# Performance work log

Measured on AMD Instinct MI355X. Metric: run time of the kernel, lower is better.

Reference implementation:

```python
import jax, jax.numpy as jnp
import numpy as np

PI = np.pi


def setup_inputs() -> dict:
    key = jax.random.key(0)
    ks = jax.random.split(key, 20)
    B, L, D = 2, 1024, 512
    TP = 16      # n_sets(4) * planes_per_set(4)
    PP = 16      # pos_planes
    MAXL = 8192
    sc = 1.0 / np.sqrt(D)
    return {
        "x": jax.random.normal(ks[0], (B, L, D), jnp.float32),
        "Wk": jax.random.normal(ks[1], (TP, D), jnp.float32) * sc,
        "bk": jnp.zeros((TP,), jnp.float32),
        "Wq": jax.random.normal(ks[2], (TP, D), jnp.float32) * sc,
        "bq": jnp.zeros((TP,), jnp.float32),
        "Wv": jax.random.normal(ks[3], (D, D), jnp.float32) * sc,
        "bv": jnp.zeros((D,), jnp.float32),
        "ln_g": jnp.ones((D,), jnp.float32),
        "ln_b": jnp.zeros((D,), jnp.float32),
        "Wo": jax.random.normal(ks[4], (D, D), jnp.float32) * sc,
        "bo": jnp.zeros((D,), jnp.float32),
        "set_w": jnp.ones((4,), jnp.float32),
        "pos_phases": jax.random.normal(ks[5], (MAXL, PP), jnp.float32) * PI,
        "pos_weight": jnp.ones((1,), jnp.float32),
        "Wg1": jax.random.normal(ks[6], (D // 2, D), jnp.float32) * sc,
        "bg1": jnp.zeros((D // 2,), jnp.float32),
        "Wg2": jax.random.normal(ks[7], (1, D // 2), jnp.float32) * np.sqrt(2.0 / D),
        "bg2": jnp.zeros((1,), jnp.float32),
    }


def reference(x, Wk, bk, Wq, bq, Wv, bv, ln_g, ln_b, Wo, bo,
              set_w, pos_phases, pos_weight, Wg1, bg1, Wg2, bg2):
    B, L, D = x.shape
    n_sets, pps = 4, 4

    # --- content phasor memory ---
    kp = jnp.tanh(x @ Wk.T + bk) * PI                       # [B,L,16]
    qp = jnp.tanh(x @ Wq.T + bq) * PI
    key_ph = jnp.exp(1j * kp).reshape(B, L, n_sets, pps)    # [B,L,S,P] c64
    qry_ph = jnp.exp(1j * qp).reshape(B, L, n_sets, pps)
    Vr = x @ Wv.T + bv                                       # [B,L,D]
    V = Vr.astype(jnp.complex64)

    bound = key_ph[..., None] * V[:, :, None, None, :]       # [B,L,S,P,D] c64
    mem = jnp.cumsum(bound, axis=1)                          # prefix-sum memory
    retr = (mem * jnp.conj(qry_ph)[..., None]).sum(axis=3).real   # [B,L,S,D]
    w = jax.nn.softmax(set_w)
    content = (retr * w[None, None, :, None]).sum(axis=2)    # [B,L,D]

    # --- positional cos/sin memory ---
    ph = pos_phases[:L]                                      # [L,PP]
    c = jnp.cos(ph)[None]                                    # [1,L,PP]
    s = jnp.sin(ph)[None]
    br = Vr[:, :, None, :] * c[..., None]                    # [B,L,PP,D]
    bi = Vr[:, :, None, :] * s[..., None]
    mr = jnp.cumsum(br, axis=1)
    mi = jnp.cumsum(bi, axis=1)
    pos = (mr * c[..., None] + mi * s[..., None]).sum(axis=2)  # [B,L,D]

    # --- gate, mix, normalize, output proj ---
    g = jax.nn.sigmoid(
        jax.nn.gelu(x @ Wg1.T + bg1, approximate=False) @ Wg2.T + bg2)  # [B,L,1]
    total = g * content + (1.0 - g) * jax.nn.sigmoid(pos_weight) * pos
    norm = jnp.sqrt(jnp.arange(1, L + 1, dtype=x.dtype) * pps)[None, :, None]
    t = total / norm
    mu = t.mean(-1, keepdims=True)
    var = ((t - mu) ** 2).mean(-1, keepdims=True)
    tn = (t - mu) / jnp.sqrt(var + 1e-5) * ln_g + ln_b
    return x + tn @ Wo.T + bo
```

## Files before the change

### kernel.cpp

```cpp
#include <hip/hip_runtime.h>
#include <math.h>

#define PI_F 3.14159265358979323846f
#define BB 2
#define LL 1024
#define NCH 64
#define CHUNK 32
#define NCHUNK (LL/CHUNK)
#define NW 1408
#define YH 384

typedef __attribute__((ext_vector_type(8))) short short8;
typedef __attribute__((ext_vector_type(4))) float floatx4;
typedef const __attribute__((address_space(1))) unsigned int cgu32;
typedef __attribute__((address_space(3))) unsigned int lu32;

__device__ __forceinline__ unsigned short f2bf(float f){
    unsigned u = __float_as_uint(f);
    unsigned r = (u + 0x7fff + ((u >> 16) & 1)) >> 16;
    return (unsigned short)r;
}

__global__ __launch_bounds__(128) void k_prep(
    const float* __restrict__ Wv, const float* __restrict__ Wg1,
    const float* __restrict__ Wk, const float* __restrict__ Wq,
    const float* __restrict__ Wo,
    const float* __restrict__ bv, const float* __restrict__ bg1,
    const float* __restrict__ bk, const float* __restrict__ bq,
    const float* __restrict__ bo, const float* __restrict__ x,
    unsigned short* __restrict__ Wb, float* __restrict__ bcat,
    unsigned short* __restrict__ xb)
{
    const int bid = blockIdx.x, tid = threadIdx.x;
    if (bid < NW){
        const int n = bid;
        const float* src = (n<512) ? Wv  + (size_t)n*512
                         : (n<768) ? Wg1 + (size_t)(n-512)*512
                         : (n<784) ? Wk  + (size_t)(n-768)*512
                         : (n<800) ? Wq  + (size_t)(n-784)*512
                         : (n<896) ? (const float*)0
                                   : Wo  + (size_t)(n-896)*512;
        float4 v = make_float4(0.f,0.f,0.f,0.f);
        if (src) v = ((const float4*)src)[tid];
        ushort4 o; o.x=f2bf(v.x); o.y=f2bf(v.y); o.z=f2bf(v.z); o.w=f2bf(v.w);
        ((ushort4*)(Wb + (size_t)n*512))[tid] = o;
        if (tid == 0)
            bcat[n] = (n<512)?bv[n] : (n<768)?bg1[n-512] : (n<784)?bk[n-768]
                    : (n<800)?bq[n-784] : (n<896)?0.f : bo[n-896];
    } else {
        const size_t i = (size_t)(bid - NW)*128 + tid;
        float4 v = ((const float4*)x)[i];
        ushort4 o; o.x=f2bf(v.x); o.y=f2bf(v.y); o.z=f2bf(v.z); o.w=f2bf(v.w);
        ((ushort4*)xb)[i] = o;
    }
}

__device__ __forceinline__ void gemm64x64(
    const unsigned short* Ag, const unsigned short* Bg,
    short* As, short* Bs, int tid, floatx4 acc[2][2])
{
    const int lane = tid & 63, w = tid >> 6;
    const int wm = w & 1, wn = w >> 1;
    const int q = lane >> 4, m15 = lane & 15;
    for (int kt = 0; kt < 512; kt += 64) {
        __syncthreads();
        #pragma unroll
        for (int i = 0; i < 2; ++i) {
            const int rowbase = (w*2 + i) * 8;
            const int r  = rowbase + (lane >> 3);
            const int gb = (lane & 7) ^ (r & 7);
            const unsigned short* ga  = Ag + (size_t)r*512 + kt + gb*8;
            const unsigned short* gbp = Bg + (size_t)r*512 + kt + gb*8;
            __builtin_amdgcn_global_load_lds((cgu32*)(const void*)ga,
                                             (lu32*)(As + rowbase*64), 16, 0, 0);
            __builtin_amdgcn_global_load_lds((cgu32*)(const void*)gbp,
                                             (lu32*)(Bs + rowbase*64), 16, 0, 0);
        }
        __syncthreads();
        #pragma unroll
        for (int k32 = 0; k32 < 64; k32 += 32) {
            short8 af[2], bf[2];
            #pragma unroll
            for (int t = 0; t < 2; ++t) {
                const int ra  = 32*wm + 16*t + m15;
                const int sba = ((k32>>3) + q) ^ (ra & 7);
                af[t] = *(const short8*)(As + ra*64 + sba*8);
                const int rb  = 32*wn + 16*t + m15;
                const int sbb = ((k32>>3) + q) ^ (rb & 7);
                bf[t] = *(const short8*)(Bs + rb*64 + sbb*8);
            }
            #pragma unroll
            for (int mt = 0; mt < 2; ++mt)
                #pragma unroll
                for (int nt = 0; nt < 2; ++nt)
                    acc[mt][nt] = __builtin_amdgcn_mfma_f32_16x16x32_bf16(
                        af[mt], bf[nt], acc[mt][nt], 0, 0, 0);
        }
    }
}

__global__ __launch_bounds__(256) void kg1(
    const unsigned short* __restrict__ xb, const unsigned short* __restrict__ Wb,
    const float* __restrict__ bcat, unsigned short* __restrict__ Vt,
    float* __restrict__ Yh)
{
    __shared__ short As[64*64], Bs[64*64];
    const int tid = threadIdx.x;
    const int row0 = blockIdx.x*64, n0 = blockIdx.y*64;
    floatx4 acc[2][2];
    #pragma unroll
    for (int mt=0;mt<2;++mt)
        #pragma unroll
        for (int nt=0;nt<2;++nt) acc[mt][nt] = (floatx4){0.f,0.f,0.f,0.f};
    gemm64x64(xb + (size_t)row0*512, Wb + (size_t)n0*512, As, Bs, tid, acc);
    const int lane = tid & 63, w = tid >> 6;
    const int wm = w & 1, wn = w >> 1, q = lane >> 4, m15 = lane & 15;
    if (n0 < 512){
        const int b = row0 >> 10, lb = row0 & 1023;
        #pragma unroll
        for (int mt=0;mt<2;++mt)
            #pragma unroll
            for (int nt=0;nt<2;++nt){
                const int d = n0 + 32*wn + 16*nt + m15;
                const float bb = bcat[d];
                const int l0 = lb + 32*wm + 16*mt + q*4;
                ushort4 o;
                o.x = f2bf(acc[mt][nt][0] + bb);
                o.y = f2bf(acc[mt][nt][1] + bb);
                o.z = f2bf(acc[mt][nt][2] + bb);
                o.w = f2bf(acc[mt][nt][3] + bb);
                *(ushort4*)(Vt + ((size_t)(b*512 + d))*1024 + l0) = o;
            }
    } else {
        #pragma unroll
        for (int mt=0;mt<2;++mt)
            #pragma unroll
            for (int nt=0;nt<2;++nt){
                const int n = n0 + 32*wn + 16*nt + m15;
                const float bb = bcat[n];
                #pragma unroll
                for (int reg=0;reg<4;++reg){
                    const int m = row0 + 32*wm + 16*mt + q*4 + reg;
                    Yh[(size_t)m*YH + (n-512)] = acc[mt][nt][reg] + bb;
                }
            }
    }
}

__global__ __launch_bounds__(256) void k_act(
    const float* __restrict__ Yh, const float* __restrict__ Wg2,
    const float* __restrict__ bg2, const float* __restrict__ set_w,
    const float* __restrict__ pos_phases, const float* __restrict__ pos_weight,
    unsigned short* __restrict__ ab, unsigned short* __restrict__ Rb,
    unsigned short* __restrict__ aT)
{
    const int tid = threadIdx.x, lane = tid & 63, w = tid >> 6;
    const int row0 = blockIdx.x * 8;
    float s0=set_w[0], s1=set_w[1], s2=set_w[2], s3=set_w[3];
    float m = fmaxf(fmaxf(s0,s1), fmaxf(s2,s3));
    float e0=expf(s0-m), e1=expf(s1-m), e2=expf(s2-m), e3=expf(s3-m);
    float esum = e0+e1+e2+e3;
    float spw = 1.f/(1.f+expf(-pos_weight[0]));
    float b2 = bg2[0];
    #pragma unroll
    for (int rr=0;rr<2;++rr){
        int row = row0 + w + 4*rr;
        const float* yrow = Yh + (size_t)row*YH;
        float hs = 0.f;
        #pragma unroll
        for (int i=0;i<4;++i){
            float hv = yrow[lane + 64*i];
            float ge = 0.5f*hv*(1.f + erff(hv*0.70710678118f));
            hs += ge * Wg2[lane + 64*i];
        }
        #pragma unroll
        for (int off=32; off; off>>=1) hs += __shfl_xor(hs, off, 64);
        float g = 1.f/(1.f+expf(-(hs + b2)));
        if (lane < 16){
            int j = lane;
            int l = row & (LL-1);
            int b = row >> 10;
            float kang = PI_F*tanhf(yrow[256 + j]);
            float qang = PI_F*tanhf(yrow[272 + j]);
            float wsm = (j<4?e0: j<8?e1: j<12?e2: e3) / esum;
            float rnorm = 1.f/(2.f*sqrtf((float)(l+1)));
            float av[4], rv[4];
            av[0] = cosf(kang); av[1] = sinf(kang);
            float cw = g*wsm*rnorm;
            rv[0] = cw*cosf(qang); rv[1] = cw*sinf(qang);
            float ph = pos_phases[(size_t)l*16 + j];
            float pc = cosf(ph), ps = sinf(ph);
            av[2] = pc; av[3] = ps;
            float cp = (1.f-g)*spw*rnorm;
            rv[2] = cp*pc; rv[3] = cp*ps;
            unsigned short* arow = ab + (size_t)row*NCH;
            unsigned short* Rrow = Rb + (size_t)row*NCH;
            #pragma unroll
            for (int t=0;t<4;++t){
                arow[16*t + j] = f2bf(av[t]);
                Rrow[16*t + j] = f2bf(rv[t]);
                aT[((size_t)b*NCH + 16*t + j)*1024 + l] = f2bf(av[t]);
            }
        }
    }
}

__global__ __launch_bounds__(256) void k2a_chunksum(
    const unsigned short* __restrict__ aT, const unsigned short* __restrict__ Vt,
    float* __restrict__ P)
{
    const int c = blockIdx.x, b = blockIdx.y, z = blockIdx.z;
    const int tid = threadIdx.x, lane = tid & 63, w = tid >> 6;
    const int q = lane >> 4, m15 = lane & 15;
    short8 af[4];
    #pragma unroll
    for (int mt=0;mt<4;++mt)
        af[mt] = *(const short8*)(aT + ((size_t)b*NCH + 16*mt + m15)*1024 + c*32 + q*8);
    floatx4 acc[4][4];
    #pragma unroll
    for (int mt=0;mt<4;++mt)
        #pragma unroll
        for (int nt=0;nt<4;++nt) acc[mt][nt] = (floatx4){0.f,0.f,0.f,0.f};
    #pragma unroll
    for (int nt=0;nt<4;++nt){
        const int d = z*256 + w*64 + 16*nt + m15;
        short8 bf = *(const short8*)(Vt + ((size_t)(b*512 + d))*1024 + c*32 + q*8);
        #pragma unroll
        for (int mt=0;mt<4;++mt)
            acc[mt][nt] = __builtin_amdgcn_mfma_f32_16x16x32_bf16(af[mt], bf, acc[mt][nt], 0,0,0);
    }
    float* Pc = P + ((size_t)(b*NCHUNK + c))*512*NCH;
    #pragma unroll
    for (int mt=0;mt<4;++mt)
        #pragma unroll
        for (int nt=0;nt<4;++nt){
            const int d = z*256 + w*64 + 16*nt + m15;
            const int ch0 = 16*mt + q*4;
            *(floatx4*)(Pc + (size_t)d*NCH + ch0) = acc[mt][nt];
        }
}

__global__ __launch_bounds__(256) void k2b_prefix(
    const float* __restrict__ P, unsigned short* __restrict__ S0t)
{
    const int b = blockIdx.y;
    const size_t idx = (size_t)blockIdx.x*256 + threadIdx.x;
    float run = 0.f;
    for (int c=0;c<NCHUNK;++c){
        const size_t o = ((size_t)(b*NCHUNK + c))*512*NCH + idx;
        float v = P[o];
        S0t[o] = f2bf(run);
        run += v;
    }
}

__global__ __launch_bounds__(256) void k2c_scan(
    const unsigned short* __restrict__ ab, const unsigned short* __restrict__ Rb,
    const unsigned short* __restrict__ Vt, const unsigned short* __restrict__ S0t,
    const float* __restrict__ ln_g, const float* __restrict__ ln_b,
    unsigned short* __restrict__ Tn)
{
    __shared__ short Msh[32*32];
    __shared__ float Tsh[32*512];
    const int c = blockIdx.x, b = blockIdx.y;
    const int tid = threadIdx.x, lane = tid & 63, w = tid >> 6;
    const int q = lane >> 4, m15 = lane & 15;
    const int grow = b*1024 + c*32;

    if (w == 0){
        floatx4 mcc[2][2];
        #pragma unroll
        for (int mt=0;mt<2;++mt)
            #pragma unroll
            for (int nt=0;nt<2;++nt) mcc[mt][nt] = (floatx4){0.f,0.f,0.f,0.f};
        #pragma unroll
        for (int ks=0;ks<2;++ks){
            short8 ra[2], bb[2];
            #pragma unroll
            for (int t=0;t<2;++t){
                ra[t] = *(const short8*)(Rb + (size_t)(grow + 16*t + m15)*NCH + ks*32 + q*8);
                bb[t] = *(const short8*)(ab + (size_t)(grow + 16*t + m15)*NCH + ks*32 + q*8);
            }
            #pragma unroll
            for (int mt=0;mt<2;++mt)
                #pragma unroll
                for (int nt=0;nt<2;++nt)
                    mcc[mt][nt] = __builtin_amdgcn_mfma_f32_16x16x32_bf16(
                        ra[mt], bb[nt], mcc[mt][nt], 0,0,0);
        }
        #pragma unroll
        for (int mt=0;mt<2;++mt)
            #pragma unroll
            for (int nt=0;nt<2;++nt){
                const int nl = 16*nt + m15;
                #pragma unroll
                for (int reg=0;reg<4;++reg){
                    const int ml = 16*mt + q*4 + reg;
                    Msh[ml*32 + nl] = (nl <= ml) ? (short)f2bf(mcc[mt][nt][reg]) : (short)0;
                }
            }
    }
    __syncthreads();

    short8 a1[2], a2[2][2];
    #pragma unroll
    for (int mt=0;mt<2;++mt){
        a1[mt] = *(const short8*)(Msh + (16*mt + m15)*32 + q*8);
        #pragma unroll
        for (int ks=0;ks<2;++ks)
            a2[ks][mt] = *(const short8*)(Rb + (size_t)(grow + 16*mt + m15)*NCH + ks*32 + q*8);
    }
    floatx4 acc[2][8];
    #pragma unroll
    for (int mt=0;mt<2;++mt)
        #pragma unroll
        for (int nt=0;nt<8;++nt) acc[mt][nt] = (floatx4){0.f,0.f,0.f,0.f};
    const unsigned short* S0c = S0t + ((size_t)(b*NCHUNK + c))*512*NCH;
    #pragma unroll
    for (int nt=0;nt<8;++nt){
        const int d = w*128 + 16*nt + m15;
        short8 b1 = *(const short8*)(Vt + ((size_t)(b*512 + d))*1024 + c*32 + q*8);
        #pragma unroll
        for (int mt=0;mt<2;++mt)
            acc[mt][nt] = __builtin_amdgcn_mfma_f32_16x16x32_bf16(a1[mt], b1, acc[mt][nt], 0,0,0);
        #pragma unroll
        for (int ks=0;ks<2;++ks){
            short8 b2 = *(const short8*)(S0c + (size_t)d*NCH + ks*32 + q*8);
            #pragma unroll
            for (int mt=0;mt<2;++mt)
                acc[mt][nt] = __builtin_amdgcn_mfma_f32_16x16x32_bf16(a2[ks][mt], b2, acc[mt][nt], 0,0,0);
        }
    }
    #pragma unroll
    for (int mt=0;mt<2;++mt)
        #pragma unroll
        for (int nt=0;nt<8;++nt){
            const int d = w*128 + 16*nt + m15;
            #pragma unroll
            for (int reg=0;reg<4;++reg)
                Tsh[(16*mt + q*4 + reg)*512 + d] = acc[mt][nt][reg];
        }
    __syncthreads();

    #pragma unroll
    for (int i=0;i<8;++i){
        const int r = w*8 + i;
        float s=0.f, sq=0.f;
        #pragma unroll
        for (int t=0;t<8;++t){
            float v = Tsh[r*512 + lane + 64*t];
            s += v; sq += v*v;
        }
        #pragma unroll
        for (int off=32; off; off>>=1){
            s += __shfl_xor(s, off, 64); sq += __shfl_xor(sq, off, 64);
        }
        float mu  = s*(1.f/512.f);
        float var = sq*(1.f/512.f) - mu*mu;
        float rsd = rsqrtf(var + 1e-5f);
        unsigned short* trow = Tn + (size_t)(grow + r)*512;
        #pragma unroll
        for (int t=0;t<8;++t){
            const int d = lane + 64*t;
            float v = (Tsh[r*512 + d] - mu)*rsd*ln_g[d] + ln_b[d];
            trow[d] = f2bf(v);
        }
    }
}

__global__ __launch_bounds__(256) void kg2(
    const unsigned short* __restrict__ Tn, const unsigned short* __restrict__ Wb,
    const float* __restrict__ bcat, const float* __restrict__ x,
    float* __restrict__ out)
{
    __shared__ short As[64*64], Bs[64*64];
    const int tid = threadIdx.x;
    const int row0 = blockIdx.x*64, n0 = blockIdx.y*64;
    floatx4 acc[2][2];
    #pragma unroll
    for (int mt=0;mt<2;++mt)
        #pragma unroll
        for (int nt=0;nt<2;++nt) acc[mt][nt] = (floatx4){0.f,0.f,0.f,0.f};
    gemm64x64(Tn + (size_t)row0*512, Wb + (size_t)(896+n0)*512, As, Bs, tid, acc);
    const int lane = tid & 63, w = tid >> 6;
    const int wm = w & 1, wn = w >> 1, q = lane >> 4, m15 = lane & 15;
    #pragma unroll
    for (int mt=0;mt<2;++mt)
        #pragma unroll
        for (int nt=0;nt<2;++nt){
            const int n = n0 + 32*wn + 16*nt + m15;
            const float bb = bcat[896 + n];
            #pragma unroll
            for (int reg=0;reg<4;++reg){
                const int m = row0 + 32*wm + 16*mt + q*4 + reg;
                out[(size_t)m*512 + n] = x[(size_t)m*512 + n] + acc[mt][nt][reg] + bb;
            }
        }
}

extern "C" void kernel_launch(void* const* d_in, const int* in_sizes, int n_in,
                              void* d_out, int out_size, void* d_ws, size_t ws_size,
                              hipStream_t stream) {
    const float* x    = (const float*)d_in[0];
    const float* Wk   = (const float*)d_in[1];
    const float* bk   = (const float*)d_in[2];
    const float* Wq   = (const float*)d_in[3];
    const float* bq   = (const float*)d_in[4];
    const float* Wv   = (const float*)d_in[5];
    const float* bv   = (const float*)d_in[6];
    const float* ln_g = (const float*)d_in[7];
    const float* ln_b = (const float*)d_in[8];
    const float* Wo   = (const float*)d_in[9];
    const float* bo   = (const float*)d_in[10];
    const float* set_w      = (const float*)d_in[11];
    const float* pos_phases = (const float*)d_in[12];
    const float* pos_weight = (const float*)d_in[13];
    const float* Wg1  = (const float*)d_in[14];
    const float* bg1  = (const float*)d_in[15];
    const float* Wg2  = (const float*)d_in[16];
    const float* bg2  = (const float*)d_in[17];
    float* out = (float*)d_out;

    float* ws   = (float*)d_ws;
    float* Yh   = ws;
    float* P    = Yh + (size_t)2048*YH;
    float* bcat = P  + (size_t)BB*NCHUNK*512*NCH;
    unsigned short* Wb  = (unsigned short*)(bcat + NW);
    unsigned short* xb  = Wb  + (size_t)NW*512;
    unsigned short* Vt  = xb  + (size_t)2048*512;
    unsigned short* ab  = Vt  + (size_t)BB*512*1024;
    unsigned short* Rb  = ab  + (size_t)2048*NCH;
    unsigned short* aT  = Rb  + (size_t)2048*NCH;
    unsigned short* S0t = aT  + (size_t)BB*NCH*1024;
    unsigned short* Tn  = S0t + (size_t)BB*NCHUNK*512*NCH;

    k_prep<<<dim3(NW + 2048), 128, 0, stream>>>(
        Wv,Wg1,Wk,Wq,Wo, bv,bg1,bk,bq,bo, x, Wb, bcat, xb);
    kg1<<<dim3(2048/64, 14), 256, 0, stream>>>(xb, Wb, bcat, Vt, Yh);
    k_act<<<dim3(2048/8), 256, 0, stream>>>(
        Yh, Wg2, bg2, set_w, pos_phases, pos_weight, ab, Rb, aT);
    k2a_chunksum<<<dim3(NCHUNK, BB, 2), 256, 0, stream>>>(aT, Vt, P);
    k2b_prefix<<<dim3(512*NCH/256, BB), 256, 0, stream>>>(P, S0t);
    k2c_scan<<<dim3(NCHUNK, BB), 256, 0, stream>>>(ab, Rb, Vt, S0t, ln_g, ln_b, Tn);
    kg2<<<dim3(2048/64, 512/64), 256, 0, stream>>>(Tn, Wb, bcat, x, out);
}
```

Baseline: 134.5 us.

## Merge scan stages into cooperative kernel and enlarge GEMM tiles to 128

The activation, chunk-sum, prefix and intra-chunk scan kernels are merged into a single cooperative kernel of 128 blocks, with grid-wide syncs between the phases. This removes several kernel launch gaps. The two bf16 GEMMs move from 64x64 to 128x128 tiles with a 4x4 MFMA accumulator per wave, which improves data reuse. In exchange the GEMMs launch far fewer blocks (112 and 64) on a GPU with many CUs, and the scan phase now runs on only 64 of the 128 blocks, so parallelism may drop.

```diff
diff --git a/kernel.cpp b/kernel.cpp
--- a/kernel.cpp
+++ b/kernel.cpp
@@ -1,5 +1,8 @@
 #include <hip/hip_runtime.h>
+#include <hip/hip_cooperative_groups.h>
 #include <math.h>
+
+namespace cg = cooperative_groups;
 
 #define PI_F 3.14159265358979323846f
 #define BB 2
@@ -55,9 +58,9 @@
     }
 }
 
-__device__ __forceinline__ void gemm64x64(
+__device__ __forceinline__ void gemm128(
     const unsigned short* Ag, const unsigned short* Bg,
-    short* As, short* Bs, int tid, floatx4 acc[2][2])
+    short* As, short* Bs, int tid, floatx4 acc[4][4])
 {
     const int lane = tid & 63, w = tid >> 6;
     const int wm = w & 1, wn = w >> 1;
@@ -65,34 +68,34 @@
     for (int kt = 0; kt < 512; kt += 64) {
         __syncthreads();
         #pragma unroll
-        for (int i = 0; i < 2; ++i) {
-            const int rowbase = (w*2 + i) * 8;
+        for (int i = 0; i < 4; ++i) {
+            const int rowbase = w*32 + i*8;
             const int r  = rowbase + (lane >> 3);
             const int gb = (lane & 7) ^ (r & 7);
-            const unsigned short* ga  = Ag + (size_t)r*512 + kt + gb*8;
-            const unsigned short* gbp = Bg + (size_t)r*512 + kt + gb*8;
-            __builtin_amdgcn_global_load_lds((cgu32*)(const void*)ga,
-                                             (lu32*)(As + rowbase*64), 16, 0, 0);
-            __builtin_amdgcn_global_load_lds((cgu32*)(const void*)gbp,
-                                             (lu32*)(Bs + rowbase*64), 16, 0, 0);
+            __builtin_amdgcn_global_load_lds(
+                (cgu32*)(const void*)(Ag + (size_t)r*512 + kt + gb*8),
+                (lu32*)(As + rowbase*64), 16, 0, 0);
+            __builtin_amdgcn_global_load_lds(
+                (cgu32*)(const void*)(Bg + (size_t)r*512 + kt + gb*8),
+                (lu32*)(Bs + rowbase*64), 16, 0, 0);
         }
         __syncthreads();
         #pragma unroll
         for (int k32 = 0; k32 < 64; k32 += 32) {
-            short8 af[2], bf[2];
-            #pragma unroll
-            for (int t = 0; t < 2; ++t) {
-                const int ra  = 32*wm + 16*t + m15;
+            short8 af[4], bf[4];
+            #pragma unroll
+            for (int t = 0; t < 4; ++t) {
+                const int ra  = 64*wm + 16*t + m15;
                 const int sba = ((k32>>3) + q) ^ (ra & 7);
                 af[t] = *(const short8*)(As + ra*64 + sba*8);
-                const int rb  = 32*wn + 16*t + m15;
+                const int rb  = 64*wn + 16*t + m15;
                 const int sbb = ((k32>>3) + q) ^ (rb & 7);
                 bf[t] = *(const short8*)(Bs + rb*64 + sbb*8);
             }
             #pragma unroll
-            for (int mt = 0; mt < 2; ++mt)
-                #pragma unroll
-                for (int nt = 0; nt < 2; ++nt)
+            for (int mt = 0; mt < 4; ++mt)
+                #pragma unroll
+                for (int nt = 0; nt < 4; ++nt)
                     acc[mt][nt] = __builtin_amdgcn_mfma_f32_16x16x32_bf16(
                         af[mt], bf[nt], acc[mt][nt], 0, 0, 0);
         }
@@ -104,26 +107,26 @@
     const float* __restrict__ bcat, unsigned short* __restrict__ Vt,
     float* __restrict__ Yh)
 {
-    __shared__ short As[64*64], Bs[64*64];
+    __shared__ short As[128*64], Bs[128*64];
     const int tid = threadIdx.x;
-    const int row0 = blockIdx.x*64, n0 = blockIdx.y*64;
-    floatx4 acc[2][2];
+    const int row0 = blockIdx.x*128, n0 = blockIdx.y*128;
+    floatx4 acc[4][4];
     #pragma unroll
-    for (int mt=0;mt<2;++mt)
-        #pragma unroll
-        for (int nt=0;nt<2;++nt) acc[mt][nt] = (floatx4){0.f,0.f,0.f,0.f};
-    gemm64x64(xb + (size_t)row0*512, Wb + (size_t)n0*512, As, Bs, tid, acc);
+    for (int mt=0;mt<4;++mt)
+        #pragma unroll
+        for (int nt=0;nt<4;++nt) acc[mt][nt] = (floatx4){0.f,0.f,0.f,0.f};
+    gemm128(xb + (size_t)row0*512, Wb + (size_t)n0*512, As, Bs, tid, acc);
     const int lane = tid & 63, w = tid >> 6;
     const int wm = w & 1, wn = w >> 1, q = lane >> 4, m15 = lane & 15;
     if (n0 < 512){
         const int b = row0 >> 10, lb = row0 & 1023;
         #pragma unroll
-        for (int mt=0;mt<2;++mt)
-            #pragma unroll
-            for (int nt=0;nt<2;++nt){
-                const int d = n0 + 32*wn + 16*nt + m15;
+        for (int mt=0;mt<4;++mt)
+            #pragma unroll
+            for (int nt=0;nt<4;++nt){
+                const int d = n0 + 64*wn + 16*nt + m15;
                 const float bb = bcat[d];
-                const int l0 = lb + 32*wm + 16*mt + q*4;
+                const int l0 = lb + 64*wm + 16*mt + q*4;
                 ushort4 o;
                 o.x = f2bf(acc[mt][nt][0] + bb);
                 o.y = f2bf(acc[mt][nt][1] + bb);
@@ -133,237 +136,237 @@
             }
     } else {
         #pragma unroll
-        for (int mt=0;mt<2;++mt)
-            #pragma unroll
-            for (int nt=0;nt<2;++nt){
-                const int n = n0 + 32*wn + 16*nt + m15;
+        for (int mt=0;mt<4;++mt)
+            #pragma unroll
+            for (int nt=0;nt<4;++nt){
+                const int n = n0 + 64*wn + 16*nt + m15;
                 const float bb = bcat[n];
                 #pragma unroll
                 for (int reg=0;reg<4;++reg){
-                    const int m = row0 + 32*wm + 16*mt + q*4 + reg;
+                    const int m = row0 + 64*wm + 16*mt + q*4 + reg;
                     Yh[(size_t)m*YH + (n-512)] = acc[mt][nt][reg] + bb;
                 }
             }
     }
 }
 
-__global__ __launch_bounds__(256) void k_act(
+__global__ __launch_bounds__(256) void k_scan(
     const float* __restrict__ Yh, const float* __restrict__ Wg2,
     const float* __restrict__ bg2, const float* __restrict__ set_w,
     const float* __restrict__ pos_phases, const float* __restrict__ pos_weight,
+    const unsigned short* __restrict__ Vt,
     unsigned short* __restrict__ ab, unsigned short* __restrict__ Rb,
-    unsigned short* __restrict__ aT)
-{
-    const int tid = threadIdx.x, lane = tid & 63, w = tid >> 6;
-    const int row0 = blockIdx.x * 8;
-    float s0=set_w[0], s1=set_w[1], s2=set_w[2], s3=set_w[3];
-    float m = fmaxf(fmaxf(s0,s1), fmaxf(s2,s3));
-    float e0=expf(s0-m), e1=expf(s1-m), e2=expf(s2-m), e3=expf(s3-m);
-    float esum = e0+e1+e2+e3;
-    float spw = 1.f/(1.f+expf(-pos_weight[0]));
-    float b2 = bg2[0];
-    #pragma unroll
-    for (int rr=0;rr<2;++rr){
-        int row = row0 + w + 4*rr;
-        const float* yrow = Yh + (size_t)row*YH;
-        float hs = 0.f;
-        #pragma unroll
-        for (int i=0;i<4;++i){
-            float hv = yrow[lane + 64*i];
-            float ge = 0.5f*hv*(1.f + erff(hv*0.70710678118f));
-            hs += ge * Wg2[lane + 64*i];
-        }
-        #pragma unroll
-        for (int off=32; off; off>>=1) hs += __shfl_xor(hs, off, 64);
-        float g = 1.f/(1.f+expf(-(hs + b2)));
-        if (lane < 16){
-            int j = lane;
-            int l = row & (LL-1);
-            int b = row >> 10;
-            float kang = PI_F*tanhf(yrow[256 + j]);
-            float qang = PI_F*tanhf(yrow[272 + j]);
-            float wsm = (j<4?e0: j<8?e1: j<12?e2: e3) / esum;
-            float rnorm = 1.f/(2.f*sqrtf((float)(l+1)));
-            float av[4], rv[4];
-            av[0] = cosf(kang); av[1] = sinf(kang);
-            float cw = g*wsm*rnorm;
-            rv[0] = cw*cosf(qang); rv[1] = cw*sinf(qang);
-            float ph = pos_phases[(size_t)l*16 + j];
-            float pc = cosf(ph), ps = sinf(ph);
-            av[2] = pc; av[3] = ps;
-            float cp = (1.f-g)*spw*rnorm;
-            rv[2] = cp*pc; rv[3] = cp*ps;
-            unsigned short* arow = ab + (size_t)row*NCH;
-            unsigned short* Rrow = Rb + (size_t)row*NCH;
-            #pragma unroll
-            for (int t=0;t<4;++t){
-                arow[16*t + j] = f2bf(av[t]);
-                Rrow[16*t + j] = f2bf(rv[t]);
-                aT[((size_t)b*NCH + 16*t + j)*1024 + l] = f2bf(av[t]);
-            }
-        }
-    }
-}
-
-__global__ __launch_bounds__(256) void k2a_chunksum(
-    const unsigned short* __restrict__ aT, const unsigned short* __restrict__ Vt,
-    float* __restrict__ P)
-{
-    const int c = blockIdx.x, b = blockIdx.y, z = blockIdx.z;
-    const int tid = threadIdx.x, lane = tid & 63, w = tid >> 6;
-    const int q = lane >> 4, m15 = lane & 15;
-    short8 af[4];
-    #pragma unroll
-    for (int mt=0;mt<4;++mt)
-        af[mt] = *(const short8*)(aT + ((size_t)b*NCH + 16*mt + m15)*1024 + c*32 + q*8);
-    floatx4 acc[4][4];
-    #pragma unroll
-    for (int mt=0;mt<4;++mt)
-        #pragma unroll
-        for (int nt=0;nt<4;++nt) acc[mt][nt] = (floatx4){0.f,0.f,0.f,0.f};
-    #pragma unroll
-    for (int nt=0;nt<4;++nt){
-        const int d = z*256 + w*64 + 16*nt + m15;
-        short8 bf = *(const short8*)(Vt + ((size_t)(b*512 + d))*1024 + c*32 + q*8);
-        #pragma unroll
-        for (int mt=0;mt<4;++mt)
-            acc[mt][nt] = __builtin_amdgcn_mfma_f32_16x16x32_bf16(af[mt], bf, acc[mt][nt], 0,0,0);
-    }
-    float* Pc = P + ((size_t)(b*NCHUNK + c))*512*NCH;
-    #pragma unroll
-    for (int mt=0;mt<4;++mt)
-        #pragma unroll
-        for (int nt=0;nt<4;++nt){
-            const int d = z*256 + w*64 + 16*nt + m15;
-            const int ch0 = 16*mt + q*4;
-            *(floatx4*)(Pc + (size_t)d*NCH + ch0) = acc[mt][nt];
-        }
-}
-
-__global__ __launch_bounds__(256) void k2b_prefix(
-    const float* __restrict__ P, unsigned short* __restrict__ S0t)
-{
-    const int b = blockIdx.y;
-    const size_t idx = (size_t)blockIdx.x*256 + threadIdx.x;
-    float run = 0.f;
-    for (int c=0;c<NCHUNK;++c){
-        const size_t o = ((size_t)(b*NCHUNK + c))*512*NCH + idx;
-        float v = P[o];
-        S0t[o] = f2bf(run);
-        run += v;
-    }
-}
-
-__global__ __launch_bounds__(256) void k2c_scan(
-    const unsigned short* __restrict__ ab, const unsigned short* __restrict__ Rb,
-    const unsigned short* __restrict__ Vt, const unsigned short* __restrict__ S0t,
+    unsigned short* __restrict__ aT, float* __restrict__ P,
+    unsigned short* __restrict__ S0t,
     const float* __restrict__ ln_g, const float* __restrict__ ln_b,
     unsigned short* __restrict__ Tn)
 {
+    __shared__ float Tsh[32*512];
     __shared__ short Msh[32*32];
-    __shared__ float Tsh[32*512];
-    const int c = blockIdx.x, b = blockIdx.y;
-    const int tid = threadIdx.x, lane = tid & 63, w = tid >> 6;
+    cg::grid_group grid = cg::this_grid();
+    const int bid = blockIdx.x, tid = threadIdx.x;
+    const int lane = tid & 63, w = tid >> 6;
     const int q = lane >> 4, m15 = lane & 15;
-    const int grow = b*1024 + c*32;
-
-    if (w == 0){
-        floatx4 mcc[2][2];
+
+    {
+        const int row0 = bid * 16;
+        float s0=set_w[0], s1=set_w[1], s2=set_w[2], s3=set_w[3];
+        float m = fmaxf(fmaxf(s0,s1), fmaxf(s2,s3));
+        float e0=expf(s0-m), e1=expf(s1-m), e2=expf(s2-m), e3=expf(s3-m);
+        float esum = e0+e1+e2+e3;
+        float spw = 1.f/(1.f+expf(-pos_weight[0]));
+        float b2 = bg2[0];
+        #pragma unroll
+        for (int rr=0;rr<4;++rr){
+            int row = row0 + w + 4*rr;
+            const float* yrow = Yh + (size_t)row*YH;
+            float hs = 0.f;
+            #pragma unroll
+            for (int i=0;i<4;++i){
+                float hv = yrow[lane + 64*i];
+                float ge = 0.5f*hv*(1.f + erff(hv*0.70710678118f));
+                hs += ge * Wg2[lane + 64*i];
+            }
+            #pragma unroll
+            for (int off=32; off; off>>=1) hs += __shfl_xor(hs, off, 64);
+            float g = 1.f/(1.f+expf(-(hs + b2)));
+            if (lane < 16){
+                int j = lane;
+                int l = row & (LL-1);
+                int b = row >> 10;
+                float kang = PI_F*tanhf(yrow[256 + j]);
+                float qang = PI_F*tanhf(yrow[272 + j]);
+                float wsm = (j<4?e0: j<8?e1: j<12?e2: e3) / esum;
+                float rnorm = 1.f/(2.f*sqrtf((float)(l+1)));
+                float av[4], rv[4];
+                av[0] = cosf(kang); av[1] = sinf(kang);
+                float cw = g*wsm*rnorm;
+                rv[0] = cw*cosf(qang); rv[1] = cw*sinf(qang);
+                float ph = pos_phases[(size_t)l*16 + j];
+                float pc = cosf(ph), ps = sinf(ph);
+                av[2] = pc; av[3] = ps;
+                float cp = (1.f-g)*spw*rnorm;
+                rv[2] = cp*pc; rv[3] = cp*ps;
+                unsigned short* arow = ab + (size_t)row*NCH;
+                unsigned short* Rrow = Rb + (size_t)row*NCH;
+                #pragma unroll
+                for (int t=0;t<4;++t){
+                    arow[16*t + j] = f2bf(av[t]);
+                    Rrow[16*t + j] = f2bf(rv[t]);
+                    aT[((size_t)b*NCH + 16*t + j)*1024 + l] = f2bf(av[t]);
+                }
+            }
+        }
+    }
+    grid.sync();
+
+    {
+        const int c = bid & 31, b = (bid >> 5) & 1, z = bid >> 6;
+        short8 af[4];
+        #pragma unroll
+        for (int mt=0;mt<4;++mt)
+            af[mt] = *(const short8*)(aT + ((size_t)b*NCH + 16*mt + m15)*1024 + c*32 + q*8);
+        floatx4 acc[4][4];
+        #pragma unroll
+        for (int mt=0;mt<4;++mt)
+            #pragma unroll
+            for (int nt=0;nt<4;++nt) acc[mt][nt] = (floatx4){0.f,0.f,0.f,0.f};
+        #pragma unroll
+        for (int nt=0;nt<4;++nt){
+            const int d = z*256 + w*64 + 16*nt + m15;
+            short8 bf = *(const short8*)(Vt + ((size_t)(b*512 + d))*1024 + c*32 + q*8);
+            #pragma unroll
+            for (int mt=0;mt<4;++mt)
+                acc[mt][nt] = __builtin_amdgcn_mfma_f32_16x16x32_bf16(af[mt], bf, acc[mt][nt], 0,0,0);
+        }
+        float* Pc = P + ((size_t)(b*NCHUNK + c))*512*NCH;
+        #pragma unroll
+        for (int mt=0;mt<4;++mt)
+            #pragma unroll
+            for (int nt=0;nt<4;++nt){
+                const int d = z*256 + w*64 + 16*nt + m15;
+                *(floatx4*)(Pc + (size_t)d*NCH + 16*mt + q*4) = acc[mt][nt];
+            }
+    }
+    grid.sync();
+
+    {
+        const size_t idx = (size_t)bid*256 + tid;
+        #pragma unroll
+        for (int b=0;b<BB;++b){
+            float run = 0.f;
+            for (int c=0;c<NCHUNK;++c){
+                const size_t o = ((size_t)(b*NCHUNK + c))*512*NCH + idx;
+                float v = P[o];
+                S0t[o] = f2bf(run);
+                run += v;
+            }
+        }
+    }
+    grid.sync();
+
+    if (bid < 64){
+        const int c = bid & 31, b = bid >> 5;
+        const int grow = b*1024 + c*32;
+
+        if (w == 0){
+            floatx4 mcc[2][2];
+            #pragma unroll
+            for (int mt=0;mt<2;++mt)
+                #pragma unroll
+                for (int nt=0;nt<2;++nt) mcc[mt][nt] = (floatx4){0.f,0.f,0.f,0.f};
+            #pragma unroll
+            for (int ks=0;ks<2;++ks){
+                short8 ra[2], bb[2];
+                #pragma unroll
+                for (int t=0;t<2;++t){
+                    ra[t] = *(const short8*)(Rb + (size_t)(grow + 16*t + m15)*NCH + ks*32 + q*8);
+                    bb[t] = *(const short8*)(ab + (size_t)(grow + 16*t + m15)*NCH + ks*32 + q*8);
+                }
+                #pragma unroll
+                for (int mt=0;mt<2;++mt)
+                    #pragma unroll
+                    for (int nt=0;nt<2;++nt)
+                        mcc[mt][nt] = __builtin_amdgcn_mfma_f32_16x16x32_bf16(
+                            ra[mt], bb[nt], mcc[mt][nt], 0,0,0);
+            }
+            #pragma unroll
+            for (int mt=0;mt<2;++mt)
+                #pragma unroll
+                for (int nt=0;nt<2;++nt){
+                    const int nl = 16*nt + m15;
+                    #pragma unroll
+                    for (int reg=0;reg<4;++reg){
+                        const int ml = 16*mt + q*4 + reg;
+                        Msh[ml*32 + nl] = (nl <= ml) ? (short)f2bf(mcc[mt][nt][reg]) : (short)0;
+                    }
+                }
+        }
+        __syncthreads();
+
+        short8 a1[2], a2[2][2];
+        #pragma unroll
+        for (int mt=0;mt<2;++mt){
+            a1[mt] = *(const short8*)(Msh + (16*mt + m15)*32 + q*8);
+            #pragma unroll
+            for (int ks=0;ks<2;++ks)
+                a2[ks][mt] = *(const short8*)(Rb + (size_t)(grow + 16*mt + m15)*NCH + ks*32 + q*8);
+        }
+        floatx4 acc[2][8];
         #pragma unroll
         for (int mt=0;mt<2;++mt)
             #pragma unroll
-            for (int nt=0;nt<2;++nt) mcc[mt][nt] = (floatx4){0.f,0.f,0.f,0.f};
-        #pragma unroll
-        for (int ks=0;ks<2;++ks){
-            short8 ra[2], bb[2];
-            #pragma unroll
-            for (int t=0;t<2;++t){
-                ra[t] = *(const short8*)(Rb + (size_t)(grow + 16*t + m15)*NCH + ks*32 + q*8);
-                bb[t] = *(const short8*)(ab + (size_t)(grow + 16*t + m15)*NCH + ks*32 + q*8);
-            }
-            #pragma unroll
-            for (int mt=0;mt<2;++mt)
-                #pragma unroll
-                for (int nt=0;nt<2;++nt)
-                    mcc[mt][nt] = __builtin_amdgcn_mfma_f32_16x16x32_bf16(
-                        ra[mt], bb[nt], mcc[mt][nt], 0,0,0);
-        }
-        #pragma unroll
-        for (int mt=0;mt<2;++mt)
-            #pragma unroll
-            for (int nt=0;nt<2;++nt){
-                const int nl = 16*nt + m15;
-                #pragma unroll
-                for (int reg=0;reg<4;++reg){
-                    const int ml = 16*mt + q*4 + reg;
-                    Msh[ml*32 + nl] = (nl <= ml) ? (short)f2bf(mcc[mt][nt][reg]) : (short)0;
-                }
-            }
-    }
-    __syncthreads();
-
-    short8 a1[2], a2[2][2];
-    #pragma unroll
-    for (int mt=0;mt<2;++mt){
-        a1[mt] = *(const short8*)(Msh + (16*mt + m15)*32 + q*8);
-        #pragma unroll
-        for (int ks=0;ks<2;++ks)
-            a2[ks][mt] = *(const short8*)(Rb + (size_t)(grow + 16*mt + m15)*NCH + ks*32 + q*8);
-    }
-    floatx4 acc[2][8];
-    #pragma unroll
-    for (int mt=0;mt<2;++mt)
-        #pragma unroll
-        for (int nt=0;nt<8;++nt) acc[mt][nt] = (floatx4){0.f,0.f,0.f,0.f};
-    const unsigned short* S0c = S0t + ((size_t)(b*NCHUNK + c))*512*NCH;
-    #pragma unroll
-    for (int nt=0;nt<8;++nt){
-        const int d = w*128 + 16*nt + m15;
-        short8 b1 = *(const short8*)(Vt + ((size_t)(b*512 + d))*1024 + c*32 + q*8);
-        #pragma unroll
-        for (int mt=0;mt<2;++mt)
-            acc[mt][nt] = __builtin_amdgcn_mfma_f32_16x16x32_bf16(a1[mt], b1, acc[mt][nt], 0,0,0);
-        #pragma unroll
-        for (int ks=0;ks<2;++ks){
-            short8 b2 = *(const short8*)(S0c + (size_t)d*NCH + ks*32 + q*8);
-            #pragma unroll
-            for (int mt=0;mt<2;++mt)
-                acc[mt][nt] = __builtin_amdgcn_mfma_f32_16x16x32_bf16(a2[ks][mt], b2, acc[mt][nt], 0,0,0);
-        }
-    }
-    #pragma unroll
-    for (int mt=0;mt<2;++mt)
+            for (int nt=0;nt<8;++nt) acc[mt][nt] = (floatx4){0.f,0.f,0.f,0.f};
+        const unsigned short* S0c = S0t + ((size_t)(b*NCHUNK + c))*512*NCH;
         #pragma unroll
         for (int nt=0;nt<8;++nt){
             const int d = w*128 + 16*nt + m15;
-            #pragma unroll
-            for (int reg=0;reg<4;++reg)
-                Tsh[(16*mt + q*4 + reg)*512 + d] = acc[mt][nt][reg];
-        }
-    __syncthreads();
-
-    #pragma unroll
-    for (int i=0;i<8;++i){
-        const int r = w*8 + i;
-        float s=0.f, sq=0.f;
-        #pragma unroll
-        for (int t=0;t<8;++t){
-            float v = Tsh[r*512 + lane + 64*t];
-            s += v; sq += v*v;
-        }
-        #pragma unroll
-        for (int off=32; off; off>>=1){
-            s += __shfl_xor(s, off, 64); sq += __shfl_xor(sq, off, 64);
-        }
-        float mu  = s*(1.f/512.f);
-        float var = sq*(1.f/512.f) - mu*mu;
-        float rsd = rsqrtf(var + 1e-5f);
-        unsigned short* trow = Tn + (size_t)(grow + r)*512;
-        #pragma unroll
-        for (int t=0;t<8;++t){
-            const int d = lane + 64*t;
-            float v = (Tsh[r*512 + d] - mu)*rsd*ln_g[d] + ln_b[d];
-            trow[d] = f2bf(v);
+            short8 b1 = *(const short8*)(Vt + ((size_t)(b*512 + d))*1024 + c*32 + q*8);
+            #pragma unroll
+            for (int mt=0;mt<2;++mt)
+                acc[mt][nt] = __builtin_amdgcn_mfma_f32_16x16x32_bf16(a1[mt], b1, acc[mt][nt], 0,0,0);
+            #pragma unroll
+            for (int ks=0;ks<2;++ks){
+                short8 b2 = *(const short8*)(S0c + (size_t)d*NCH + ks*32 + q*8);
+                #pragma unroll
+                for (int mt=0;mt<2;++mt)
+                    acc[mt][nt] = __builtin_amdgcn_mfma_f32_16x16x32_bf16(a2[ks][mt], b2, acc[mt][nt], 0,0,0);
+            }
+        }
+        #pragma unroll
+        for (int mt=0;mt<2;++mt)
+            #pragma unroll
+            for (int nt=0;nt<8;++nt){
+                const int d = w*128 + 16*nt + m15;
+                #pragma unroll
+                for (int reg=0;reg<4;++reg)
+                    Tsh[(16*mt + q*4 + reg)*512 + d] = acc[mt][nt][reg];
+            }
+        __syncthreads();
+
+        #pragma unroll
+        for (int i=0;i<8;++i){
+            const int r = w*8 + i;
+            float s=0.f, sq=0.f;
+            #pragma unroll
+            for (int t=0;t<8;++t){
+                float v = Tsh[r*512 + lane + 64*t];
+                s += v; sq += v*v;
+            }
+            #pragma unroll
+            for (int off=32; off; off>>=1){
+                s += __shfl_xor(s, off, 64); sq += __shfl_xor(sq, off, 64);
+            }
+            float mu  = s*(1.f/512.f);
+            float var = sq*(1.f/512.f) - mu*mu;
+            float rsd = rsqrtf(var + 1e-5f);
+            unsigned short* trow = Tn + (size_t)(grow + r)*512;
+            #pragma unroll
+            for (int t=0;t<8;++t){
+                const int d = lane + 64*t;
+                float v = (Tsh[r*512 + d] - mu)*rsd*ln_g[d] + ln_b[d];
+                trow[d] = f2bf(v);
+            }
         }
     }
 }
@@ -373,26 +376,26 @@
     const float* __restrict__ bcat, const float* __restrict__ x,
     float* __restrict__ out)
 {
-    __shared__ short As[64*64], Bs[64*64];
+    __shared__ short As[128*64], Bs[128*64];
     const int tid = threadIdx.x;
-    const int row0 = blockIdx.x*64, n0 = blockIdx.y*64;
-    floatx4 acc[2][2];
+    const int row0 = blockIdx.x*128, n0 = blockIdx.y*128;
+    floatx4 acc[4][4];
     #pragma unroll
-    for (int mt=0;mt<2;++mt)
-        #pragma unroll
-        for (int nt=0;nt<2;++nt) acc[mt][nt] = (floatx4){0.f,0.f,0.f,0.f};
-    gemm64x64(Tn + (size_t)row0*512, Wb + (size_t)(896+n0)*512, As, Bs, tid, acc);
+    for (int mt=0;mt<4;++mt)
+        #pragma unroll
+        for (int nt=0;nt<4;++nt) acc[mt][nt] = (floatx4){0.f,0.f,0.f,0.f};
+    gemm128(Tn + (size_t)row0*512, Wb + (size_t)(896+n0)*512, As, Bs, tid, acc);
     const int lane = tid & 63, w = tid >> 6;
     const int wm = w & 1, wn = w >> 1, q = lane >> 4, m15 = lane & 15;
     #pragma unroll
-    for (int mt=0;mt<2;++mt)
-        #pragma unroll
-        for (int nt=0;nt<2;++nt){
-            const int n = n0 + 32*wn + 16*nt + m15;
+    for (int mt=0;mt<4;++mt)
+        #pragma unroll
+        for (int nt=0;nt<4;++nt){
+            const int n = n0 + 64*wn + 16*nt + m15;
             const float bb = bcat[896 + n];
             #pragma unroll
             for (int reg=0;reg<4;++reg){
-                const int m = row0 + 32*wm + 16*mt + q*4 + reg;
+                const int m = row0 + 64*wm + 16*mt + q*4 + reg;
                 out[(size_t)m*512 + n] = x[(size_t)m*512 + n] + acc[mt][nt][reg] + bb;
             }
         }
@@ -436,11 +439,16 @@
 
     k_prep<<<dim3(NW + 2048), 128, 0, stream>>>(
         Wv,Wg1,Wk,Wq,Wo, bv,bg1,bk,bq,bo, x, Wb, bcat, xb);
-    kg1<<<dim3(2048/64, 14), 256, 0, stream>>>(xb, Wb, bcat, Vt, Yh);
-    k_act<<<dim3(2048/8), 256, 0, stream>>>(
-        Yh, Wg2, bg2, set_w, pos_phases, pos_weight, ab, Rb, aT);
-    k2a_chunksum<<<dim3(NCHUNK, BB, 2), 256, 0, stream>>>(aT, Vt, P);
-    k2b_prefix<<<dim3(512*NCH/256, BB), 256, 0, stream>>>(P, S0t);
-    k2c_scan<<<dim3(NCHUNK, BB), 256, 0, stream>>>(ab, Rb, Vt, S0t, ln_g, ln_b, Tn);
-    kg2<<<dim3(2048/64, 512/64), 256, 0, stream>>>(Tn, Wb, bcat, x, out);
-}
+    kg1<<<dim3(2048/128, 7), 256, 0, stream>>>(xb, Wb, bcat, Vt, Yh);
+    {
+        void* args[] = {
+            (void*)&Yh, (void*)&Wg2, (void*)&bg2, (void*)&set_w,
+            (void*)&pos_phases, (void*)&pos_weight, (void*)&Vt,
+            (void*)&ab, (void*)&Rb, (void*)&aT, (void*)&P, (void*)&S0t,
+            (void*)&ln_g, (void*)&ln_b, (void*)&Tn
+        };
+        hipLaunchCooperativeKernel((const void*)k_scan, dim3(128), dim3(256),
+                                   args, 0, stream);
+    }
+    kg2<<<dim3(2048/128, 4), 256, 0, stream>>>(Tn, Wb, bcat, x, out);
+}
```

Measured after the change: 235.2 us. 74.8% more time.
